# Optimization experiments

Hardware: AMD Instinct MI355X
Metric: run time of the kernel (lower is better)

The kernel has to match this reference:

```python
import jax, jax.numpy as jnp
import numpy as np

IH, IW = 32, 32
HEADS, DIM_HEAD = 8, 32
EPS = 1e-6


def conv3x3(x, w):
    # x: [B,C,H,W], w: [O,I,3,3], stride 1, pad 1, no bias
    return jax.lax.conv_general_dilated(x, w, (1, 1), ((1, 1), (1, 1)),
                                        dimension_numbers=('NCHW', 'OIHW', 'NCHW'))


def groupnorm1(x, g, b):
    # GroupNorm(1, C): normalize over (C,H,W) per sample
    mu = jnp.mean(x, axis=(1, 2, 3), keepdims=True)
    var = jnp.var(x, axis=(1, 2, 3), keepdims=True)
    xn = (x - mu) * jax.lax.rsqrt(var + EPS)
    return xn * g[None, :, None, None] + b[None, :, None, None]


def proj(x, w, g, b):
    return jax.nn.gelu(groupnorm1(conv3x3(x, w), g, b), approximate=False)


def relative_index(ih, iw):
    coords = np.stack(np.meshgrid(np.arange(ih), np.arange(iw), indexing='ij')).reshape(2, -1)
    rel = coords[:, :, None] - coords[:, None, :]  # [2, n, n]
    rel[0] += ih - 1
    rel[1] += iw - 1
    rel[0] *= 2 * iw - 1
    return jnp.asarray(rel.sum(0).reshape(-1))  # [n*n]


def setup_inputs() -> dict:
    key = jax.random.key(0)
    ks = jax.random.split(key, 9)
    C = HEADS * DIM_HEAD  # 256
    B = 8
    s = 0.02
    inp = {
        'x': jax.random.normal(ks[0], (B, C, IH, IW), jnp.float32),
        'wq': jax.random.normal(ks[1], (C, C, 3, 3), jnp.float32) * s,
        'wk': jax.random.normal(ks[2], (C, C, 3, 3), jnp.float32) * s,
        'wv': jax.random.normal(ks[3], (C, C, 3, 3), jnp.float32) * s,
        'gq': jnp.ones((C,), jnp.float32), 'bq': jnp.zeros((C,), jnp.float32),
        'gk': jnp.ones((C,), jnp.float32), 'bk': jnp.zeros((C,), jnp.float32),
        'gv': jnp.ones((C,), jnp.float32), 'bv': jnp.zeros((C,), jnp.float32),
        'bias_table': jax.random.normal(ks[4], ((2 * IH - 1) * (2 * IW - 1), HEADS), jnp.float32) * s,
        'wo': jax.random.normal(ks[5], (C, C), jnp.float32) * s,
        'bo': jnp.zeros((C,), jnp.float32),
    }
    return inp


def reference(x, wq, wk, wv, gq, bq, gk, bk, gv, bv, bias_table, wo, bo):
    B, C, ih, iw = x.shape
    n = ih * iw
    h, d = HEADS, DIM_HEAD

    q = proj(x, wq, gq, bq)  # [B,C,H,W]
    k = proj(x, wk, gk, bk)
    v = proj(x, wv, gv, bv)

    # 'b c ih iw -> b (ih iw) c' then 'b n (h d) -> b h n d'  ==  [B,h,d,n] -> [B,h,n,d]
    def to_heads(t):
        return t.reshape(B, h, d, n).transpose(0, 1, 3, 2)

    q4, k4, v4 = to_heads(q), to_heads(k), to_heads(v)

    # NOTE: original code applies self.scale only when y is not None; y=None here -> no scale.
    dots = jnp.einsum('bhnd,bhmd->bhnm', q4, k4)  # [B,h,n,n]

    rel_idx = relative_index(ih, iw)  # [n*n]
    rel_bias = bias_table[rel_idx].reshape(n, n, h).transpose(2, 0, 1)[None]  # [1,h,n,n]

    attn = jax.nn.softmax(dots + rel_bias, axis=-1)
    out = jnp.einsum('bhnm,bhmd->bhnd', attn, v4)  # [B,h,n,d]

    # 'b h n d -> b n (h d)' then 'b (ih iw) c -> b c ih iw'
    out = out.transpose(0, 2, 1, 3).reshape(B, n, C).transpose(0, 2, 1).reshape(B, C, ih, iw)

    # to_out: 1x1 conv with bias (dropout=0 in eval)
    out = jnp.einsum('oc,bchw->bohw', wo, out) + bo[None, :, None, None]
    return out
```

## Files before the change

kernel.cpp:

```cpp
#include <hip/hip_runtime.h>
#include <cstdint>
#include <cstddef>

#define GEPS 1e-6f

using bf16x8 = __attribute__((ext_vector_type(8))) short;
using f32x4  = __attribute__((ext_vector_type(4))) float;

__device__ inline ushort f2bf(float x) {
    union { float f; uint32_t u; } v; v.f = x;
    uint32_t r = (v.u + 0x7fffu + ((v.u >> 16) & 1u)) >> 16;
    return (ushort)r;
}
__device__ inline float bf2f(ushort b) {
    union { float f; uint32_t u; } v; v.u = ((uint32_t)b) << 16;
    return v.f;
}

__device__ inline void gll16(const void* g, void* l) {
    __builtin_amdgcn_global_load_lds(
        (const __attribute__((address_space(1))) void*)g,
        (__attribute__((address_space(3))) void*)l, 16, 0, 0);
}

__global__ __launch_bounds__(256) void prep_k(
    const float* __restrict__ x,
    const float* __restrict__ wq, const float* __restrict__ wk,
    const float* __restrict__ wv, const float* __restrict__ wo,
    const float* __restrict__ btab,
    ushort* __restrict__ Xcl, ushort* __restrict__ Wbuf,
    ushort* __restrict__ wo_bf, ushort* __restrict__ Bx)
{
    __shared__ __align__(16) ushort Xs[3 * 34 * 128];
    int tid = threadIdx.x;
    int blk = blockIdx.x;

    if (blk < 256) {
        int b = blk >> 5, y = blk & 31;
#pragma unroll
        for (int it = 0; it < 8; ++it) {
            int idx = it * 256 + tid;
            int ci = idx >> 3, pxg = idx & 7;
            float4 v = *(const float4*)&x[((size_t)(b * 256 + ci)) * 1024 + y * 32 + pxg * 4];
            int base = (pxg * 4) * 264 + ci;
            Xs[base + 0 * 264] = f2bf(v.x);
            Xs[base + 1 * 264] = f2bf(v.y);
            Xs[base + 2 * 264] = f2bf(v.z);
            Xs[base + 3 * 264] = f2bf(v.w);
        }
        __syncthreads();
        uint4 z4 = make_uint4(0u, 0u, 0u, 0u);
        ushort* orow = Xcl + ((size_t)(b * 34) + y + 1) * 34 * 256;
#pragma unroll
        for (int it = 0; it < 4; ++it) {
            int idx = it * 256 + tid;
            int px = idx >> 5, ci8 = idx & 31;
            *(uint4*)&orow[(px + 1) * 256 + ci8 * 8] =
                *(const uint4*)&Xs[px * 264 + ci8 * 8];
        }
        if (tid < 64) {
            int side = tid >> 5, ci8 = tid & 31;
            *(uint4*)&orow[side * 33 * 256 + ci8 * 8] = z4;
        }
        if (y == 0 || y == 31) {
            ushort* zrow = Xcl + ((size_t)(b * 34) + (y == 0 ? 0 : 33)) * 34 * 256;
#pragma unroll
            for (int it = 0; it < 5; ++it) {
                int idx = it * 256 + tid;
                if (idx < 1088) *(uint4*)&zrow[idx * 8] = z4;
            }
        }
        return;
    }
    if (blk < 1024) {
        int wrow = blk - 256;
        int proj = wrow >> 8, co = wrow & 255;
        const float* src = ((proj == 0) ? wq : ((proj == 1) ? wk : wv)) + (size_t)co * 2304;
#pragma unroll
        for (int j = 0; j < 9; ++j) {
            int idx = j * 256 + tid;
            Xs[idx] = f2bf(src[idx]);
        }
        __syncthreads();
        ushort* dst = Wbuf + (size_t)wrow * 2304;
#pragma unroll
        for (int j = 0; j < 9; ++j)
            dst[j * 256 + tid] = Xs[tid * 9 + j];
        return;
    }
    if (blk < 1088) {
        int t = (blk - 1024) * 256 + tid;
        float4 v = *(const float4*)&wo[(size_t)t * 4];
        union { uint2 u; ushort s[4]; } o;
        o.s[0] = f2bf(v.x); o.s[1] = f2bf(v.y); o.s[2] = f2bf(v.z); o.s[3] = f2bf(v.w);
        *(uint2*)&wo_bf[(size_t)t * 4] = o.u;
        return;
    }
    int g = (blk - 1088) * 4 + (tid >> 6);
    int l = tid & 63;
    int h = g >> 10, qt = (g >> 4) & 63, kt = g & 15;
    int quad = l >> 4, c = l & 15;
    union { uint4 v[2]; ushort s[16]; } o;
#pragma unroll
    for (int f = 0; f < 4; ++f)
#pragma unroll
        for (int r = 0; r < 4; ++r) {
            int qrow = qt * 16 + quad * 4 + r;
            int key = kt * 64 + f * 16 + c;
            int dy = (qrow >> 5) - (key >> 5) + 31;
            int dx = (qrow & 31) - (key & 31) + 31;
            o.s[f * 4 + r] = f2bf(btab[(dy * 63 + dx) * 8 + h]);
        }
    uint4* dst = (uint4*)(Bx + ((size_t)g * 64 + l) * 16);
    dst[0] = o.v[0];
    dst[1] = o.v[1];
}

__global__ __launch_bounds__(256, 3) void gemm_bt(
    const ushort* __restrict__ A, const ushort* __restrict__ B,
    int M, int N, int K,
    ushort* __restrict__ Cpart,
    float* __restrict__ Cout, const float* __restrict__ bias, int mode)
{
    __shared__ __align__(16) ushort As[128 * 64];
    __shared__ __align__(16) ushort Bs[128 * 64];
    int tid = threadIdx.x;
    int mbase = blockIdx.x * 128, nbase = blockIdx.y * 128;
    int kspan = K / gridDim.z;
    int k0 = blockIdx.z * kspan;
    int wave = tid >> 6, lane = tid & 63;
    int wm = wave & 1, wn = wave >> 1;
    int quad = lane >> 4, c = lane & 15;

    int row_s = tid >> 3;
    int cc8 = (tid & 7) ^ (row_s & 7);
    ushort* ldsA = As + wave * 512;
    ushort* ldsB = Bs + wave * 512;

    int rb[4];
    if (mode == 0) {
#pragma unroll
        for (int R = 0; R < 4; ++R) {
            int r = mbase + R * 32 + row_s;
            int b_ = r >> 10, yy = (r >> 5) & 31, xx = r & 31;
            rb[R] = ((b_ * 34 + yy) * 34 + xx) * 256;
        }
    }

    f32x4 acc[4][4];
#pragma unroll
    for (int i = 0; i < 4; ++i)
#pragma unroll
        for (int j = 0; j < 4; ++j) acc[i][j] = (f32x4){0.f, 0.f, 0.f, 0.f};

    for (int kb = k0; kb < k0 + kspan; kb += 64) {
        __syncthreads();
        if (mode == 0) {
            int tap = kb >> 8;
            int kh = (tap * 11) >> 5;
            int kw = tap - kh * 3;
            int toff = (kh * 34 + kw) * 256 + (kb & 255) + cc8 * 8;
#pragma unroll
            for (int R = 0; R < 4; ++R) {
                gll16(A + rb[R] + toff, ldsA + R * 2048);
                gll16(B + (size_t)(nbase + R * 32 + row_s) * K + kb + cc8 * 8,
                      ldsB + R * 2048);
            }
        } else {
#pragma unroll
            for (int R = 0; R < 4; ++R) {
                int row = R * 32 + row_s;
                gll16(A + (size_t)(mbase + row) * K + kb + cc8 * 8,
                      ldsA + R * 2048);
                gll16(B + (size_t)(nbase + row) * K + kb + cc8 * 8,
                      ldsB + R * 2048);
            }
        }
        __syncthreads();
#pragma unroll
        for (int kq = 0; kq < 2; ++kq) {
            bf16x8 af[4], bfr[4];
            int sw = ((kq * 4 + quad) ^ (c & 7)) * 8;
#pragma unroll
            for (int i = 0; i < 4; ++i) {
                af[i]  = *(const bf16x8*)&As[(wm * 64 + i * 16 + c) * 64 + sw];
                bfr[i] = *(const bf16x8*)&Bs[(wn * 64 + i * 16 + c) * 64 + sw];
            }
#pragma unroll
            for (int i = 0; i < 4; ++i)
#pragma unroll
                for (int j = 0; j < 4; ++j)
                    acc[i][j] = __builtin_amdgcn_mfma_f32_16x16x32_bf16(
                        af[i], bfr[j], acc[i][j], 0, 0, 0);
        }
    }

    if (mode == 0) {
        ushort* Cp = Cpart + (size_t)blockIdx.z * M * N;
#pragma unroll
        for (int i = 0; i < 4; ++i) {
            int mrow = mbase + wm * 64 + i * 16 + quad * 4;
#pragma unroll
            for (int j = 0; j < 4; ++j) {
                int ncol = nbase + wn * 64 + j * 16 + c;
#pragma unroll
                for (int r = 0; r < 4; ++r)
                    Cp[(size_t)(mrow + r) * N + ncol] = f2bf(acc[i][j][r]);
            }
        }
    } else {
#pragma unroll
        for (int i = 0; i < 4; ++i) {
            int mrow0 = mbase + wm * 64 + i * 16 + quad * 4;
#pragma unroll
            for (int j = 0; j < 4; ++j) {
                int ncol = nbase + wn * 64 + j * 16 + c;
                int bb = ncol >> 10, px = ncol & 1023;
#pragma unroll
                for (int r = 0; r < 4; ++r) {
                    int o = mrow0 + r;
                    Cout[((size_t)bb * 256 + o) * 1024 + px] = acc[i][j][r] + bias[o];
                }
            }
        }
    }
}

__global__ __launch_bounds__(256) void stats1_k(const ushort* __restrict__ P0,
                                                const ushort* __restrict__ P1,
                                                float2* __restrict__ part)
{
    int t = blockIdx.x * 256 + threadIdx.x;
    size_t base = (size_t)t * 8;
    union { uint4 v; ushort s[8]; } a, b2;
    a.v  = *(const uint4*)&P0[base];
    b2.v = *(const uint4*)&P1[base];
    float s1 = 0.f, s2 = 0.f;
#pragma unroll
    for (int e = 0; e < 8; ++e) {
        float v = bf2f(a.s[e]) + bf2f(b2.s[e]);
        s1 += v; s2 += v * v;
    }
#pragma unroll
    for (int mk = 1; mk < 32; mk <<= 1) {
        s1 += __shfl_xor(s1, mk, 64);
        s2 += __shfl_xor(s2, mk, 64);
    }
    if ((threadIdx.x & 31) == 0) {
        int gg = t >> 5;
        int m = gg / 3;
        int proj = gg - m * 3;
        int b = m >> 10, slot = m & 1023;
        part[(proj * 8 + b) * 1024 + slot] = make_float2(s1, s2);
    }
}

__global__ __launch_bounds__(256) void stats2_k(const float2* __restrict__ part,
                                                float* __restrict__ stats)
{
    __shared__ float w1[4], w2[4];
    int s = blockIdx.x, tid = threadIdx.x;
    float s1 = 0.f, s2 = 0.f;
#pragma unroll
    for (int i = 0; i < 4; ++i) {
        float2 v = part[(size_t)s * 1024 + tid * 4 + i];
        s1 += v.x; s2 += v.y;
    }
#pragma unroll
    for (int mk = 1; mk < 64; mk <<= 1) {
        s1 += __shfl_xor(s1, mk, 64);
        s2 += __shfl_xor(s2, mk, 64);
    }
    if ((tid & 63) == 0) { w1[tid >> 6] = s1; w2[tid >> 6] = s2; }
    __syncthreads();
    if (tid == 0) {
        stats[s * 2 + 0] = w1[0] + w1[1] + w1[2] + w1[3];
        stats[s * 2 + 1] = w2[0] + w2[1] + w2[2] + w2[3];
    }
}

__global__ void gn_k(const ushort* __restrict__ P0, const ushort* __restrict__ P1,
                     const float* __restrict__ stats,
                     const float* __restrict__ gq, const float* __restrict__ bq,
                     const float* __restrict__ gk, const float* __restrict__ bk,
                     const float* __restrict__ gv, const float* __restrict__ bv,
                     ushort* __restrict__ qb, ushort* __restrict__ kb2,
                     ushort* __restrict__ vx)
{
    int t = blockIdx.x * 256 + threadIdx.x;
    int m = t / 96;
    int nn = (t - m * 96) * 8;
    int proj = nn >> 8, co = nn & 255;
    int b = m >> 10, px = m & 1023;
    float s1 = stats[(proj * 8 + b) * 2 + 0];
    float s2 = stats[(proj * 8 + b) * 2 + 1];
    const float Ninv = 1.f / 262144.f;
    float mu = s1 * Ninv;
    float var = fmaxf(s2 * Ninv - mu * mu, 0.f);
    float rsig = rsqrtf(var + GEPS);
    const float* gam = (proj == 0) ? gq : ((proj == 1) ? gk : gv);
    const float* bet = (proj == 0) ? bq : ((proj == 1) ? bk : bv);

    size_t base = (size_t)m * 768 + nn;
    union { uint4 v; ushort s[8]; } a, c2;
    a.v  = *(const uint4*)&P0[base];
    c2.v = *(const uint4*)&P1[base];
    union { uint4 v; ushort s[8]; } outp;
#pragma unroll
    for (int e = 0; e < 8; ++e) {
        int cc = co + e;
        float xv = bf2f(a.s[e]) + bf2f(c2.s[e]);
        float xn = (xv - mu) * rsig * gam[cc] + bet[cc];
        float ge = 0.5f * xn * (1.f + erff(xn * 0.70710678118654752f));
        outp.s[e] = f2bf(ge);
    }
    int h = co >> 5, d = co & 31;
    if (proj == 0) {
        *(uint4*)(qb + ((((size_t)b * 8 + h) * 1024 + px) * 32 + d)) = outp.v;
    } else if (proj == 1) {
        *(uint4*)(kb2 + ((((size_t)b * 8 + h) * 1024 + px) * 32 + d)) = outp.v;
    } else {
        ushort* vb = vx + ((size_t)b * 8 + h) * 32768;
        int kca = px >> 5, quad = (px >> 3) & 3, j = px & 7;
#pragma unroll
        for (int e = 0; e < 8; ++e) {
            int dd = d + e;
            vb[(((kca * 2 + (dd >> 4)) * 64) + quad * 16 + (dd & 15)) * 8 + j] = outp.s[e];
        }
    }
}

__global__ __launch_bounds__(256, 8) void attn_k(
    const ushort* __restrict__ qb, const ushort* __restrict__ kb,
    const ushort* __restrict__ vx, const ushort* __restrict__ Bx,
    ushort* __restrict__ Opart, float* __restrict__ lpart)
{
    __shared__ __align__(16) ushort Pl[4 * 16 * 72];
    int tid = threadIdx.x, wave = tid >> 6, lane = tid & 63;
    int quad = lane >> 4, c = lane & 15;
    int bh = blockIdx.y;
    int h = bh & 7;
    int z = blockIdx.z;
    int qbase = blockIdx.x * 64 + wave * 16;

    const ushort* Q  = qb + (size_t)bh * 1024 * 32;
    const ushort* Kp = kb + (size_t)bh * 1024 * 32;
    const ushort* Vb = vx + (size_t)bh * 32768;
    const ushort* bxp = Bx + (((size_t)(h * 64 + (qbase >> 4)) * 16) * 64 + lane) * 16;
    ushort* Pw = Pl + wave * 16 * 72;

    bf16x8 qf = *(const bf16x8*)&Q[(qbase + c) * 32 + quad * 8];

    float l_[4] = {0.f, 0.f, 0.f, 0.f};
    f32x4 Of0 = {0.f, 0.f, 0.f, 0.f}, Of1 = {0.f, 0.f, 0.f, 0.f};

    for (int kb64 = z * 512; kb64 < z * 512 + 512; kb64 += 64) {
        f32x4 S[4];
        f32x4 zf = {0.f, 0.f, 0.f, 0.f};
#pragma unroll
        for (int f = 0; f < 4; ++f) {
            bf16x8 kf = *(const bf16x8*)&Kp[(kb64 + f * 16 + c) * 32 + quad * 8];
            S[f] = __builtin_amdgcn_mfma_f32_16x16x32_bf16(qf, kf, zf, 0, 0, 0);
        }
        union { uint4 v[2]; ushort s[16]; } bu;
        const uint4* bsrc = (const uint4*)(bxp + (size_t)(kb64 >> 6) * 1024);
        bu.v[0] = bsrc[0];
        bu.v[1] = bsrc[1];
#pragma unroll
        for (int f = 0; f < 4; ++f)
#pragma unroll
            for (int r = 0; r < 4; ++r) {
                float p = __expf(S[f][r] + bf2f(bu.s[f * 4 + r]));
                S[f][r] = p;
                l_[r] += p;
            }
#pragma unroll
        for (int f = 0; f < 4; ++f)
#pragma unroll
            for (int r = 0; r < 4; ++r)
                Pw[(quad * 4 + r) * 72 + f * 16 + c] = f2bf(S[f][r]);
#pragma unroll
        for (int kc = 0; kc < 2; ++kc) {
            int kca = (kb64 >> 5) + kc;
            bf16x8 pf = *(const bf16x8*)&Pw[c * 72 + kc * 32 + quad * 8];
            bf16x8 vf0 = *(const bf16x8*)&Vb[((kca * 2 + 0) * 64 + lane) * 8];
            Of0 = __builtin_amdgcn_mfma_f32_16x16x32_bf16(pf, vf0, Of0, 0, 0, 0);
            bf16x8 vf1 = *(const bf16x8*)&Vb[((kca * 2 + 1) * 64 + lane) * 8];
            Of1 = __builtin_amdgcn_mfma_f32_16x16x32_bf16(pf, vf1, Of1, 0, 0, 0);
        }
    }
#pragma unroll
    for (int r = 0; r < 4; ++r) {
        float l = l_[r];
        l += __shfl_xor(l, 1, 64);
        l += __shfl_xor(l, 2, 64);
        l += __shfl_xor(l, 4, 64);
        l += __shfl_xor(l, 8, 64);
        int qr = qbase + quad * 4 + r;
        size_t ob = (((size_t)z * 64 + bh) * 1024 + qr) * 32;
        Opart[ob + c]      = f2bf(Of0[r]);
        Opart[ob + 16 + c] = f2bf(Of1[r]);
        if (c == 0) lpart[(size_t)z * 65536 + bh * 1024 + qr] = l;
    }
}

__global__ __launch_bounds__(256) void combine_k(const ushort* __restrict__ Opart,
                                                 const float* __restrict__ lpart,
                                                 ushort* __restrict__ attnout)
{
    int t = blockIdx.x * 256 + threadIdx.x;
    int g = t & 3;
    int qg = t >> 2;
    int bh = qg >> 10, qr = qg & 1023;
    int b = bh >> 3, h = bh & 7;
    size_t ob = ((size_t)qg) * 32 + g * 8;
    union { uint4 v; ushort s[8]; } o0, o1;
    o0.v = *(const uint4*)&Opart[ob];
    o1.v = *(const uint4*)&Opart[(size_t)64 * 1024 * 32 + ob];
    float inv = 1.f / (lpart[qg] + lpart[65536 + qg]);
    union { uint4 u; ushort s[8]; } o;
#pragma unroll
    for (int e = 0; e < 8; ++e)
        o.s[e] = f2bf((bf2f(o0.s[e]) + bf2f(o1.s[e])) * inv);
    *(uint4*)&attnout[(((size_t)b * 1024 + qr) * 256) + h * 32 + g * 8] = o.u;
}

extern "C" void kernel_launch(void* const* d_in, const int* in_sizes, int n_in,
                              void* d_out, int out_size, void* d_ws, size_t ws_size,
                              hipStream_t stream)
{
    const float* x    = (const float*)d_in[0];
    const float* wq   = (const float*)d_in[1];
    const float* wk   = (const float*)d_in[2];
    const float* wv   = (const float*)d_in[3];
    const float* gq   = (const float*)d_in[4];
    const float* bq   = (const float*)d_in[5];
    const float* gk   = (const float*)d_in[6];
    const float* bk   = (const float*)d_in[7];
    const float* gv   = (const float*)d_in[8];
    const float* bv   = (const float*)d_in[9];
    const float* btab = (const float*)d_in[10];
    const float* wo   = (const float*)d_in[11];
    const float* bo   = (const float*)d_in[12];
    float* out = (float*)d_out;

    char* w = (char*)d_ws;
    size_t off = 0;
    auto alloc = [&](size_t bytes) -> char* {
        char* p = w + off;
        off += (bytes + 255) & ~(size_t)255;
        return p;
    };
    ushort* Xcl     = (ushort*)alloc(8ull * 34 * 34 * 256 * 2);
    ushort* Wbuf    = (ushort*)alloc(768ull * 2304 * 2);
    ushort* wo_bf   = (ushort*)alloc(65536ull * 2);
    ushort* Bx      = (ushort*)alloc(8192ull * 64 * 16 * 2);
    ushort* P0      = (ushort*)alloc(8192ull * 768 * 2);
    ushort* P1      = (ushort*)alloc(8192ull * 768 * 2);
    float2* part    = (float2*)alloc(48ull * 1024 * 8);
    float*  stats   = (float*)alloc(384);
    ushort* Opart   = (ushort*)alloc(2ull * 64 * 1024 * 32 * 2);
    float*  lpart   = (float*)alloc(2ull * 64 * 1024 * 4);
    ushort* qb      = (ushort*)alloc(8ull * 8 * 1024 * 32 * 2);
    ushort* kb2     = (ushort*)alloc(8ull * 8 * 1024 * 32 * 2);
    ushort* vx      = (ushort*)alloc(8ull * 8 * 32 * 1024 * 2);
    ushort* attnout = (ushort*)alloc(8ull * 1024 * 256 * 2);

    prep_k<<<3136, 256, 0, stream>>>(x, wq, wk, wv, wo, btab,
                                     Xcl, Wbuf, wo_bf, Bx);
    gemm_bt<<<dim3(64, 6, 2), 256, 0, stream>>>(Xcl, Wbuf, 8192, 768, 2304,
                                                P0, nullptr, nullptr, 0);
    stats1_k<<<3072, 256, 0, stream>>>(P0, P1, part);
    stats2_k<<<48, 256, 0, stream>>>(part, stats);
    gn_k<<<3072, 256, 0, stream>>>(P0, P1, stats, gq, bq, gk, bk, gv, bv,
                                   qb, kb2, vx);
    attn_k<<<dim3(16, 64, 2), 256, 0, stream>>>(qb, kb2, vx, Bx, Opart, lpart);
    combine_k<<<1024, 256, 0, stream>>>(Opart, lpart, attnout);
    gemm_bt<<<dim3(2, 64, 1), 256, 0, stream>>>(wo_bf, attnout, 256, 8192, 256,
                                                nullptr, out, bo, 1);
}
```

Measured before the change: 213.0 us.

## Drop split-K in conv GEMM and attention, fuse GroupNorm stats via atomics

The conv GEMM no longer splits K across two partial buffers. It uses a 128x64 tile with twice as many N blocks and accumulates GroupNorm sums with per-block atomics in its epilogue, which removes the stats1/stats2 kernels and the second partial read in gn_k. Attention no longer splits keys into two halves, so it normalizes and writes the final output directly and the combine kernel goes away. This cuts launches and intermediate traffic, at the cost of halving grid parallelism for attention and adding float atomics, which make the statistics order-dependent.

```diff
diff --git a/kernel.cpp b/kernel.cpp
--- a/kernel.cpp
+++ b/kernel.cpp
@@ -29,7 +29,8 @@
     const float* __restrict__ wv, const float* __restrict__ wo,
     const float* __restrict__ btab,
     ushort* __restrict__ Xcl, ushort* __restrict__ Wbuf,
-    ushort* __restrict__ wo_bf, ushort* __restrict__ Bx)
+    ushort* __restrict__ wo_bf, ushort* __restrict__ Bx,
+    float* __restrict__ stats)
 {
     __shared__ __align__(16) ushort Xs[3 * 34 * 128];
     int tid = threadIdx.x;
@@ -89,6 +90,7 @@
         return;
     }
     if (blk < 1088) {
+        if (blk == 1024 && tid < 192) stats[tid] = 0.f;
         int t = (blk - 1024) * 256 + tid;
         float4 v = *(const float4*)&wo[(size_t)t * 4];
         union { uint2 u; ushort s[4]; } o;
@@ -119,15 +121,14 @@
 __global__ __launch_bounds__(256, 3) void gemm_bt(
     const ushort* __restrict__ A, const ushort* __restrict__ B,
     int M, int N, int K,
-    ushort* __restrict__ Cpart,
+    ushort* __restrict__ Cpart, float* __restrict__ stats,
     float* __restrict__ Cout, const float* __restrict__ bias, int mode)
 {
     __shared__ __align__(16) ushort As[128 * 64];
-    __shared__ __align__(16) ushort Bs[128 * 64];
+    __shared__ __align__(16) ushort Bs[64 * 64];
+    __shared__ float red[8];
     int tid = threadIdx.x;
-    int mbase = blockIdx.x * 128, nbase = blockIdx.y * 128;
-    int kspan = K / gridDim.z;
-    int k0 = blockIdx.z * kspan;
+    int mbase = blockIdx.x * 128, nbase = blockIdx.y * 64;
     int wave = tid >> 6, lane = tid & 63;
     int wm = wave & 1, wn = wave >> 1;
     int quad = lane >> 4, c = lane & 15;
@@ -147,13 +148,13 @@
         }
     }
 
-    f32x4 acc[4][4];
+    f32x4 acc[4][2];
 #pragma unroll
     for (int i = 0; i < 4; ++i)
 #pragma unroll
-        for (int j = 0; j < 4; ++j) acc[i][j] = (f32x4){0.f, 0.f, 0.f, 0.f};
-
-    for (int kb = k0; kb < k0 + kspan; kb += 64) {
+        for (int j = 0; j < 2; ++j) acc[i][j] = (f32x4){0.f, 0.f, 0.f, 0.f};
+
+    for (int kb = 0; kb < K; kb += 64) {
         __syncthreads();
         if (mode == 0) {
             int tap = kb >> 8;
@@ -161,60 +162,77 @@
             int kw = tap - kh * 3;
             int toff = (kh * 34 + kw) * 256 + (kb & 255) + cc8 * 8;
 #pragma unroll
-            for (int R = 0; R < 4; ++R) {
+            for (int R = 0; R < 4; ++R)
                 gll16(A + rb[R] + toff, ldsA + R * 2048);
-                gll16(B + (size_t)(nbase + R * 32 + row_s) * K + kb + cc8 * 8,
-                      ldsB + R * 2048);
-            }
+#pragma unroll
+            for (int S = 0; S < 2; ++S)
+                gll16(B + (size_t)(nbase + S * 32 + row_s) * K + kb + cc8 * 8,
+                      ldsB + S * 2048);
         } else {
 #pragma unroll
-            for (int R = 0; R < 4; ++R) {
-                int row = R * 32 + row_s;
-                gll16(A + (size_t)(mbase + row) * K + kb + cc8 * 8,
+            for (int R = 0; R < 4; ++R)
+                gll16(A + (size_t)(mbase + R * 32 + row_s) * K + kb + cc8 * 8,
                       ldsA + R * 2048);
-                gll16(B + (size_t)(nbase + row) * K + kb + cc8 * 8,
-                      ldsB + R * 2048);
-            }
+#pragma unroll
+            for (int S = 0; S < 2; ++S)
+                gll16(B + (size_t)(nbase + S * 32 + row_s) * K + kb + cc8 * 8,
+                      ldsB + S * 2048);
         }
         __syncthreads();
 #pragma unroll
         for (int kq = 0; kq < 2; ++kq) {
-            bf16x8 af[4], bfr[4];
+            bf16x8 af[4], bfr[2];
             int sw = ((kq * 4 + quad) ^ (c & 7)) * 8;
 #pragma unroll
-            for (int i = 0; i < 4; ++i) {
+            for (int i = 0; i < 4; ++i)
                 af[i]  = *(const bf16x8*)&As[(wm * 64 + i * 16 + c) * 64 + sw];
-                bfr[i] = *(const bf16x8*)&Bs[(wn * 64 + i * 16 + c) * 64 + sw];
-            }
+#pragma unroll
+            for (int j = 0; j < 2; ++j)
+                bfr[j] = *(const bf16x8*)&Bs[(wn * 32 + j * 16 + c) * 64 + sw];
 #pragma unroll
             for (int i = 0; i < 4; ++i)
 #pragma unroll
-                for (int j = 0; j < 4; ++j)
+                for (int j = 0; j < 2; ++j)
                     acc[i][j] = __builtin_amdgcn_mfma_f32_16x16x32_bf16(
                         af[i], bfr[j], acc[i][j], 0, 0, 0);
         }
     }
 
     if (mode == 0) {
-        ushort* Cp = Cpart + (size_t)blockIdx.z * M * N;
+        float s1 = 0.f, s2 = 0.f;
 #pragma unroll
         for (int i = 0; i < 4; ++i) {
             int mrow = mbase + wm * 64 + i * 16 + quad * 4;
 #pragma unroll
-            for (int j = 0; j < 4; ++j) {
-                int ncol = nbase + wn * 64 + j * 16 + c;
-#pragma unroll
-                for (int r = 0; r < 4; ++r)
-                    Cp[(size_t)(mrow + r) * N + ncol] = f2bf(acc[i][j][r]);
+            for (int j = 0; j < 2; ++j) {
+                int ncol = nbase + wn * 32 + j * 16 + c;
+#pragma unroll
+                for (int r = 0; r < 4; ++r) {
+                    float v = acc[i][j][r];
+                    s1 += v; s2 += v * v;
+                    Cpart[(size_t)(mrow + r) * N + ncol] = f2bf(v);
+                }
             }
+        }
+#pragma unroll
+        for (int mk = 1; mk < 64; mk <<= 1) {
+            s1 += __shfl_xor(s1, mk, 64);
+            s2 += __shfl_xor(s2, mk, 64);
+        }
+        if (lane == 0) { red[wave] = s1; red[4 + wave] = s2; }
+        __syncthreads();
+        if (tid == 0) {
+            int key = (blockIdx.y >> 2) * 8 + (blockIdx.x >> 3);
+            atomicAdd(&stats[key * 2 + 0], red[0] + red[1] + red[2] + red[3]);
+            atomicAdd(&stats[key * 2 + 1], red[4] + red[5] + red[6] + red[7]);
         }
     } else {
 #pragma unroll
         for (int i = 0; i < 4; ++i) {
             int mrow0 = mbase + wm * 64 + i * 16 + quad * 4;
 #pragma unroll
-            for (int j = 0; j < 4; ++j) {
-                int ncol = nbase + wn * 64 + j * 16 + c;
+            for (int j = 0; j < 2; ++j) {
+                int ncol = nbase + wn * 32 + j * 16 + c;
                 int bb = ncol >> 10, px = ncol & 1023;
 #pragma unroll
                 for (int r = 0; r < 4; ++r) {
@@ -226,60 +244,7 @@
     }
 }
 
-__global__ __launch_bounds__(256) void stats1_k(const ushort* __restrict__ P0,
-                                                const ushort* __restrict__ P1,
-                                                float2* __restrict__ part)
-{
-    int t = blockIdx.x * 256 + threadIdx.x;
-    size_t base = (size_t)t * 8;
-    union { uint4 v; ushort s[8]; } a, b2;
-    a.v  = *(const uint4*)&P0[base];
-    b2.v = *(const uint4*)&P1[base];
-    float s1 = 0.f, s2 = 0.f;
-#pragma unroll
-    for (int e = 0; e < 8; ++e) {
-        float v = bf2f(a.s[e]) + bf2f(b2.s[e]);
-        s1 += v; s2 += v * v;
-    }
-#pragma unroll
-    for (int mk = 1; mk < 32; mk <<= 1) {
-        s1 += __shfl_xor(s1, mk, 64);
-        s2 += __shfl_xor(s2, mk, 64);
-    }
-    if ((threadIdx.x & 31) == 0) {
-        int gg = t >> 5;
-        int m = gg / 3;
-        int proj = gg - m * 3;
-        int b = m >> 10, slot = m & 1023;
-        part[(proj * 8 + b) * 1024 + slot] = make_float2(s1, s2);
-    }
-}
-
-__global__ __launch_bounds__(256) void stats2_k(const float2* __restrict__ part,
-                                                float* __restrict__ stats)
-{
-    __shared__ float w1[4], w2[4];
-    int s = blockIdx.x, tid = threadIdx.x;
-    float s1 = 0.f, s2 = 0.f;
-#pragma unroll
-    for (int i = 0; i < 4; ++i) {
-        float2 v = part[(size_t)s * 1024 + tid * 4 + i];
-        s1 += v.x; s2 += v.y;
-    }
-#pragma unroll
-    for (int mk = 1; mk < 64; mk <<= 1) {
-        s1 += __shfl_xor(s1, mk, 64);
-        s2 += __shfl_xor(s2, mk, 64);
-    }
-    if ((tid & 63) == 0) { w1[tid >> 6] = s1; w2[tid >> 6] = s2; }
-    __syncthreads();
-    if (tid == 0) {
-        stats[s * 2 + 0] = w1[0] + w1[1] + w1[2] + w1[3];
-        stats[s * 2 + 1] = w2[0] + w2[1] + w2[2] + w2[3];
-    }
-}
-
-__global__ void gn_k(const ushort* __restrict__ P0, const ushort* __restrict__ P1,
+__global__ void gn_k(const ushort* __restrict__ P0,
                      const float* __restrict__ stats,
                      const float* __restrict__ gq, const float* __restrict__ bq,
                      const float* __restrict__ gk, const float* __restrict__ bk,
@@ -302,14 +267,13 @@
     const float* bet = (proj == 0) ? bq : ((proj == 1) ? bk : bv);
 
     size_t base = (size_t)m * 768 + nn;
-    union { uint4 v; ushort s[8]; } a, c2;
-    a.v  = *(const uint4*)&P0[base];
-    c2.v = *(const uint4*)&P1[base];
+    union { uint4 v; ushort s[8]; } a;
+    a.v = *(const uint4*)&P0[base];
     union { uint4 v; ushort s[8]; } outp;
 #pragma unroll
     for (int e = 0; e < 8; ++e) {
         int cc = co + e;
-        float xv = bf2f(a.s[e]) + bf2f(c2.s[e]);
+        float xv = bf2f(a.s[e]);
         float xn = (xv - mu) * rsig * gam[cc] + bet[cc];
         float ge = 0.5f * xn * (1.f + erff(xn * 0.70710678118654752f));
         outp.s[e] = f2bf(ge);
@@ -333,14 +297,13 @@
 __global__ __launch_bounds__(256, 8) void attn_k(
     const ushort* __restrict__ qb, const ushort* __restrict__ kb,
     const ushort* __restrict__ vx, const ushort* __restrict__ Bx,
-    ushort* __restrict__ Opart, float* __restrict__ lpart)
+    ushort* __restrict__ attnout)
 {
     __shared__ __align__(16) ushort Pl[4 * 16 * 72];
     int tid = threadIdx.x, wave = tid >> 6, lane = tid & 63;
     int quad = lane >> 4, c = lane & 15;
     int bh = blockIdx.y;
     int h = bh & 7;
-    int z = blockIdx.z;
     int qbase = blockIdx.x * 64 + wave * 16;
 
     const ushort* Q  = qb + (size_t)bh * 1024 * 32;
@@ -354,7 +317,7 @@
     float l_[4] = {0.f, 0.f, 0.f, 0.f};
     f32x4 Of0 = {0.f, 0.f, 0.f, 0.f}, Of1 = {0.f, 0.f, 0.f, 0.f};
 
-    for (int kb64 = z * 512; kb64 < z * 512 + 512; kb64 += 64) {
+    for (int kb64 = 0; kb64 < 1024; kb64 += 64) {
         f32x4 S[4];
         f32x4 zf = {0.f, 0.f, 0.f, 0.f};
 #pragma unroll
@@ -389,6 +352,7 @@
             Of1 = __builtin_amdgcn_mfma_f32_16x16x32_bf16(pf, vf1, Of1, 0, 0, 0);
         }
     }
+    int b = bh >> 3;
 #pragma unroll
     for (int r = 0; r < 4; ++r) {
         float l = l_[r];
@@ -396,33 +360,12 @@
         l += __shfl_xor(l, 2, 64);
         l += __shfl_xor(l, 4, 64);
         l += __shfl_xor(l, 8, 64);
+        float inv = 1.f / l;
         int qr = qbase + quad * 4 + r;
-        size_t ob = (((size_t)z * 64 + bh) * 1024 + qr) * 32;
-        Opart[ob + c]      = f2bf(Of0[r]);
-        Opart[ob + 16 + c] = f2bf(Of1[r]);
-        if (c == 0) lpart[(size_t)z * 65536 + bh * 1024 + qr] = l;
-    }
-}
-
-__global__ __launch_bounds__(256) void combine_k(const ushort* __restrict__ Opart,
-                                                 const float* __restrict__ lpart,
-                                                 ushort* __restrict__ attnout)
-{
-    int t = blockIdx.x * 256 + threadIdx.x;
-    int g = t & 3;
-    int qg = t >> 2;
-    int bh = qg >> 10, qr = qg & 1023;
-    int b = bh >> 3, h = bh & 7;
-    size_t ob = ((size_t)qg) * 32 + g * 8;
-    union { uint4 v; ushort s[8]; } o0, o1;
-    o0.v = *(const uint4*)&Opart[ob];
-    o1.v = *(const uint4*)&Opart[(size_t)64 * 1024 * 32 + ob];
-    float inv = 1.f / (lpart[qg] + lpart[65536 + qg]);
-    union { uint4 u; ushort s[8]; } o;
-#pragma unroll
-    for (int e = 0; e < 8; ++e)
-        o.s[e] = f2bf((bf2f(o0.s[e]) + bf2f(o1.s[e])) * inv);
-    *(uint4*)&attnout[(((size_t)b * 1024 + qr) * 256) + h * 32 + g * 8] = o.u;
+        ushort* dst = attnout + ((size_t)b * 1024 + qr) * 256 + h * 32;
+        dst[c]      = f2bf(Of0[r] * inv);
+        dst[16 + c] = f2bf(Of1[r] * inv);
+    }
 }
 
 extern "C" void kernel_launch(void* const* d_in, const int* in_sizes, int n_in,
@@ -456,26 +399,19 @@
     ushort* wo_bf   = (ushort*)alloc(65536ull * 2);
     ushort* Bx      = (ushort*)alloc(8192ull * 64 * 16 * 2);
     ushort* P0      = (ushort*)alloc(8192ull * 768 * 2);
-    ushort* P1      = (ushort*)alloc(8192ull * 768 * 2);
-    float2* part    = (float2*)alloc(48ull * 1024 * 8);
-    float*  stats   = (float*)alloc(384);
-    ushort* Opart   = (ushort*)alloc(2ull * 64 * 1024 * 32 * 2);
-    float*  lpart   = (float*)alloc(2ull * 64 * 1024 * 4);
+    float*  stats   = (float*)alloc(768);
     ushort* qb      = (ushort*)alloc(8ull * 8 * 1024 * 32 * 2);
     ushort* kb2     = (ushort*)alloc(8ull * 8 * 1024 * 32 * 2);
     ushort* vx      = (ushort*)alloc(8ull * 8 * 32 * 1024 * 2);
     ushort* attnout = (ushort*)alloc(8ull * 1024 * 256 * 2);
 
     prep_k<<<3136, 256, 0, stream>>>(x, wq, wk, wv, wo, btab,
-                                     Xcl, Wbuf, wo_bf, Bx);
-    gemm_bt<<<dim3(64, 6, 2), 256, 0, stream>>>(Xcl, Wbuf, 8192, 768, 2304,
-                                                P0, nullptr, nullptr, 0);
-    stats1_k<<<3072, 256, 0, stream>>>(P0, P1, part);
-    stats2_k<<<48, 256, 0, stream>>>(part, stats);
-    gn_k<<<3072, 256, 0, stream>>>(P0, P1, stats, gq, bq, gk, bk, gv, bv,
+                                     Xcl, Wbuf, wo_bf, Bx, stats);
+    gemm_bt<<<dim3(64, 12, 1), 256, 0, stream>>>(Xcl, Wbuf, 8192, 768, 2304,
+                                                 P0, stats, nullptr, nullptr, 0);
+    gn_k<<<3072, 256, 0, stream>>>(P0, stats, gq, bq, gk, bk, gv, bv,
                                    qb, kb2, vx);
-    attn_k<<<dim3(16, 64, 2), 256, 0, stream>>>(qb, kb2, vx, Bx, Opart, lpart);
-    combine_k<<<1024, 256, 0, stream>>>(Opart, lpart, attnout);
-    gemm_bt<<<dim3(2, 64, 1), 256, 0, stream>>>(wo_bf, attnout, 256, 8192, 256,
-                                                nullptr, out, bo, 1);
-}
+    attn_k<<<dim3(16, 64, 1), 256, 0, stream>>>(qb, kb2, vx, Bx, attnout);
+    gemm_bt<<<dim3(2, 128, 1), 256, 0, stream>>>(wo_bf, attnout, 256, 8192, 256,
+                                                 nullptr, nullptr, out, bo, 1);
+}
```

Result: slower. 230.2 us (+8.1%).

## Index relative-position bias from LDS table, fuse GN stats via atomics, narrow out-proj tiles

Applied to the files above, without the earlier changes.

Replaces the precomputed expanded bias tensor (8 heads x 1024x1024 bf16) with a compact per-head bf16 bias table. Each attention block loads the table into LDS and indexes it by relative offset. This removes a large bias write in prep and the matching global reads in attention. GroupNorm statistics are accumulated with atomics into a buffer zeroed in prep, which drops the second reduction kernel. The output-projection GEMM is templated to a narrower N tile, doubling its grid for better occupancy. The trade-offs are atomic contention, nondeterministic summation order, and possible LDS bank conflicts on the bias lookups.

```diff
diff --git a/kernel.cpp b/kernel.cpp
--- a/kernel.cpp
+++ b/kernel.cpp
@@ -29,7 +29,8 @@
     const float* __restrict__ wv, const float* __restrict__ wo,
     const float* __restrict__ btab,
     ushort* __restrict__ Xcl, ushort* __restrict__ Wbuf,
-    ushort* __restrict__ wo_bf, ushort* __restrict__ Bx)
+    ushort* __restrict__ wo_bf, ushort* __restrict__ btab_bf,
+    float* __restrict__ stats)
 {
     __shared__ __align__(16) ushort Xs[3 * 34 * 128];
     int tid = threadIdx.x;
@@ -89,6 +90,7 @@
         return;
     }
     if (blk < 1088) {
+        if (blk == 1024 && tid < 192) stats[tid] = 0.f;
         int t = (blk - 1024) * 256 + tid;
         float4 v = *(const float4*)&wo[(size_t)t * 4];
         union { uint2 u; ushort s[4]; } o;
@@ -96,36 +98,26 @@
         *(uint2*)&wo_bf[(size_t)t * 4] = o.u;
         return;
     }
-    int g = (blk - 1088) * 4 + (tid >> 6);
-    int l = tid & 63;
-    int h = g >> 10, qt = (g >> 4) & 63, kt = g & 15;
-    int quad = l >> 4, c = l & 15;
-    union { uint4 v[2]; ushort s[16]; } o;
-#pragma unroll
-    for (int f = 0; f < 4; ++f)
-#pragma unroll
-        for (int r = 0; r < 4; ++r) {
-            int qrow = qt * 16 + quad * 4 + r;
-            int key = kt * 64 + f * 16 + c;
-            int dy = (qrow >> 5) - (key >> 5) + 31;
-            int dx = (qrow & 31) - (key & 31) + 31;
-            o.s[f * 4 + r] = f2bf(btab[(dy * 63 + dx) * 8 + h]);
-        }
-    uint4* dst = (uint4*)(Bx + ((size_t)g * 64 + l) * 16);
-    dst[0] = o.v[0];
-    dst[1] = o.v[1];
-}
-
+    int idx = (blk - 1088) * 256 + tid;
+    if (idx < 31752) {
+        int h = idx / 3969;
+        int j = idx - h * 3969;
+        btab_bf[h * 4096 + j] = f2bf(btab[(size_t)j * 8 + h]);
+    }
+}
+
+template<int NF>
 __global__ __launch_bounds__(256, 3) void gemm_bt(
     const ushort* __restrict__ A, const ushort* __restrict__ B,
     int M, int N, int K,
     ushort* __restrict__ Cpart,
     float* __restrict__ Cout, const float* __restrict__ bias, int mode)
 {
+    constexpr int BN = NF * 32;
     __shared__ __align__(16) ushort As[128 * 64];
-    __shared__ __align__(16) ushort Bs[128 * 64];
+    __shared__ __align__(16) ushort Bs[BN * 64];
     int tid = threadIdx.x;
-    int mbase = blockIdx.x * 128, nbase = blockIdx.y * 128;
+    int mbase = blockIdx.x * 128, nbase = blockIdx.y * BN;
     int kspan = K / gridDim.z;
     int k0 = blockIdx.z * kspan;
     int wave = tid >> 6, lane = tid & 63;
@@ -147,11 +139,11 @@
         }
     }
 
-    f32x4 acc[4][4];
+    f32x4 acc[4][NF];
 #pragma unroll
     for (int i = 0; i < 4; ++i)
 #pragma unroll
-        for (int j = 0; j < 4; ++j) acc[i][j] = (f32x4){0.f, 0.f, 0.f, 0.f};
+        for (int j = 0; j < NF; ++j) acc[i][j] = (f32x4){0.f, 0.f, 0.f, 0.f};
 
     for (int kb = k0; kb < k0 + kspan; kb += 64) {
         __syncthreads();
@@ -161,35 +153,37 @@
             int kw = tap - kh * 3;
             int toff = (kh * 34 + kw) * 256 + (kb & 255) + cc8 * 8;
 #pragma unroll
-            for (int R = 0; R < 4; ++R) {
+            for (int R = 0; R < 4; ++R)
                 gll16(A + rb[R] + toff, ldsA + R * 2048);
-                gll16(B + (size_t)(nbase + R * 32 + row_s) * K + kb + cc8 * 8,
-                      ldsB + R * 2048);
-            }
+#pragma unroll
+            for (int S = 0; S < NF; ++S)
+                gll16(B + (size_t)(nbase + S * 32 + row_s) * K + kb + cc8 * 8,
+                      ldsB + S * 2048);
         } else {
 #pragma unroll
-            for (int R = 0; R < 4; ++R) {
-                int row = R * 32 + row_s;
-                gll16(A + (size_t)(mbase + row) * K + kb + cc8 * 8,
+            for (int R = 0; R < 4; ++R)
+                gll16(A + (size_t)(mbase + R * 32 + row_s) * K + kb + cc8 * 8,
                       ldsA + R * 2048);
-                gll16(B + (size_t)(nbase + row) * K + kb + cc8 * 8,
-                      ldsB + R * 2048);
-            }
+#pragma unroll
+            for (int S = 0; S < NF; ++S)
+                gll16(B + (size_t)(nbase + S * 32 + row_s) * K + kb + cc8 * 8,
+                      ldsB + S * 2048);
         }
         __syncthreads();
 #pragma unroll
         for (int kq = 0; kq < 2; ++kq) {
-            bf16x8 af[4], bfr[4];
+            bf16x8 af[4], bfr[NF];
             int sw = ((kq * 4 + quad) ^ (c & 7)) * 8;
 #pragma unroll
-            for (int i = 0; i < 4; ++i) {
+            for (int i = 0; i < 4; ++i)
                 af[i]  = *(const bf16x8*)&As[(wm * 64 + i * 16 + c) * 64 + sw];
-                bfr[i] = *(const bf16x8*)&Bs[(wn * 64 + i * 16 + c) * 64 + sw];
-            }
+#pragma unroll
+            for (int j = 0; j < NF; ++j)
+                bfr[j] = *(const bf16x8*)&Bs[(wn * (NF * 16) + j * 16 + c) * 64 + sw];
 #pragma unroll
             for (int i = 0; i < 4; ++i)
 #pragma unroll
-                for (int j = 0; j < 4; ++j)
+                for (int j = 0; j < NF; ++j)
                     acc[i][j] = __builtin_amdgcn_mfma_f32_16x16x32_bf16(
                         af[i], bfr[j], acc[i][j], 0, 0, 0);
         }
@@ -201,8 +195,8 @@
         for (int i = 0; i < 4; ++i) {
             int mrow = mbase + wm * 64 + i * 16 + quad * 4;
 #pragma unroll
-            for (int j = 0; j < 4; ++j) {
-                int ncol = nbase + wn * 64 + j * 16 + c;
+            for (int j = 0; j < NF; ++j) {
+                int ncol = nbase + wn * (NF * 16) + j * 16 + c;
 #pragma unroll
                 for (int r = 0; r < 4; ++r)
                     Cp[(size_t)(mrow + r) * N + ncol] = f2bf(acc[i][j][r]);
@@ -213,8 +207,8 @@
         for (int i = 0; i < 4; ++i) {
             int mrow0 = mbase + wm * 64 + i * 16 + quad * 4;
 #pragma unroll
-            for (int j = 0; j < 4; ++j) {
-                int ncol = nbase + wn * 64 + j * 16 + c;
+            for (int j = 0; j < NF; ++j) {
+                int ncol = nbase + wn * (NF * 16) + j * 16 + c;
                 int bb = ncol >> 10, px = ncol & 1023;
 #pragma unroll
                 for (int r = 0; r < 4; ++r) {
@@ -228,7 +222,7 @@
 
 __global__ __launch_bounds__(256) void stats1_k(const ushort* __restrict__ P0,
                                                 const ushort* __restrict__ P1,
-                                                float2* __restrict__ part)
+                                                float* __restrict__ stats)
 {
     int t = blockIdx.x * 256 + threadIdx.x;
     size_t base = (size_t)t * 8;
@@ -250,32 +244,9 @@
         int gg = t >> 5;
         int m = gg / 3;
         int proj = gg - m * 3;
-        int b = m >> 10, slot = m & 1023;
-        part[(proj * 8 + b) * 1024 + slot] = make_float2(s1, s2);
-    }
-}
-
-__global__ __launch_bounds__(256) void stats2_k(const float2* __restrict__ part,
-                                                float* __restrict__ stats)
-{
-    __shared__ float w1[4], w2[4];
-    int s = blockIdx.x, tid = threadIdx.x;
-    float s1 = 0.f, s2 = 0.f;
-#pragma unroll
-    for (int i = 0; i < 4; ++i) {
-        float2 v = part[(size_t)s * 1024 + tid * 4 + i];
-        s1 += v.x; s2 += v.y;
-    }
-#pragma unroll
-    for (int mk = 1; mk < 64; mk <<= 1) {
-        s1 += __shfl_xor(s1, mk, 64);
-        s2 += __shfl_xor(s2, mk, 64);
-    }
-    if ((tid & 63) == 0) { w1[tid >> 6] = s1; w2[tid >> 6] = s2; }
-    __syncthreads();
-    if (tid == 0) {
-        stats[s * 2 + 0] = w1[0] + w1[1] + w1[2] + w1[3];
-        stats[s * 2 + 1] = w2[0] + w2[1] + w2[2] + w2[3];
+        int b = m >> 10;
+        atomicAdd(&stats[(proj * 8 + b) * 2 + 0], s1);
+        atomicAdd(&stats[(proj * 8 + b) * 2 + 1], s2);
     }
 }
 
@@ -332,10 +303,11 @@
 
 __global__ __launch_bounds__(256, 8) void attn_k(
     const ushort* __restrict__ qb, const ushort* __restrict__ kb,
-    const ushort* __restrict__ vx, const ushort* __restrict__ Bx,
+    const ushort* __restrict__ vx, const ushort* __restrict__ btab_bf,
     ushort* __restrict__ Opart, float* __restrict__ lpart)
 {
     __shared__ __align__(16) ushort Pl[4 * 16 * 72];
+    __shared__ __align__(16) ushort Bh[4096];
     int tid = threadIdx.x, wave = tid >> 6, lane = tid & 63;
     int quad = lane >> 4, c = lane & 15;
     int bh = blockIdx.y;
@@ -346,10 +318,22 @@
     const ushort* Q  = qb + (size_t)bh * 1024 * 32;
     const ushort* Kp = kb + (size_t)bh * 1024 * 32;
     const ushort* Vb = vx + (size_t)bh * 32768;
-    const ushort* bxp = Bx + (((size_t)(h * 64 + (qbase >> 4)) * 16) * 64 + lane) * 16;
     ushort* Pw = Pl + wave * 16 * 72;
 
+    {
+        const ushort* src = btab_bf + (h << 12);
+#pragma unroll
+        for (int rr = 0; rr < 2; ++rr)
+            gll16(src + (rr * 256 + tid) * 8, Bh + (rr * 256 + wave * 64) * 8);
+    }
+
     bf16x8 qf = *(const bf16x8*)&Q[(qbase + c) * 32 + quad * 8];
+
+    int qy = qbase >> 5;
+    int qx0 = (qbase & 31) + quad * 4;
+    int bb = (qy + 31 - z * 16) * 63 + qx0 + 31 - c;
+
+    __syncthreads();
 
     float l_[4] = {0.f, 0.f, 0.f, 0.f};
     f32x4 Of0 = {0.f, 0.f, 0.f, 0.f}, Of1 = {0.f, 0.f, 0.f, 0.f};
@@ -362,18 +346,17 @@
             bf16x8 kf = *(const bf16x8*)&Kp[(kb64 + f * 16 + c) * 32 + quad * 8];
             S[f] = __builtin_amdgcn_mfma_f32_16x16x32_bf16(qf, kf, zf, 0, 0, 0);
         }
-        union { uint4 v[2]; ushort s[16]; } bu;
-        const uint4* bsrc = (const uint4*)(bxp + (size_t)(kb64 >> 6) * 1024);
-        bu.v[0] = bsrc[0];
-        bu.v[1] = bsrc[1];
-#pragma unroll
-        for (int f = 0; f < 4; ++f)
+#pragma unroll
+        for (int f = 0; f < 4; ++f) {
+            int ao = bb - (f >> 1) * 63 - (f & 1) * 16;
 #pragma unroll
             for (int r = 0; r < 4; ++r) {
-                float p = __expf(S[f][r] + bf2f(bu.s[f * 4 + r]));
+                float p = __expf(S[f][r] + bf2f(Bh[ao + r]));
                 S[f][r] = p;
                 l_[r] += p;
             }
+        }
+        bb -= 126;
 #pragma unroll
         for (int f = 0; f < 4; ++f)
 #pragma unroll
@@ -454,11 +437,10 @@
     ushort* Xcl     = (ushort*)alloc(8ull * 34 * 34 * 256 * 2);
     ushort* Wbuf    = (ushort*)alloc(768ull * 2304 * 2);
     ushort* wo_bf   = (ushort*)alloc(65536ull * 2);
-    ushort* Bx      = (ushort*)alloc(8192ull * 64 * 16 * 2);
-    ushort* P0      = (ushort*)alloc(8192ull * 768 * 2);
-    ushort* P1      = (ushort*)alloc(8192ull * 768 * 2);
-    float2* part    = (float2*)alloc(48ull * 1024 * 8);
-    float*  stats   = (float*)alloc(384);
+    ushort* btab_bf = (ushort*)alloc(8ull * 4096 * 2);
+    ushort* P0      = (ushort*)alloc(2ull * 8192 * 768 * 2);
+    ushort* P1      = P0 + 8192ull * 768;
+    float*  stats   = (float*)alloc(768);
     ushort* Opart   = (ushort*)alloc(2ull * 64 * 1024 * 32 * 2);
     float*  lpart   = (float*)alloc(2ull * 64 * 1024 * 4);
     ushort* qb      = (ushort*)alloc(8ull * 8 * 1024 * 32 * 2);
@@ -466,16 +448,15 @@
     ushort* vx      = (ushort*)alloc(8ull * 8 * 32 * 1024 * 2);
     ushort* attnout = (ushort*)alloc(8ull * 1024 * 256 * 2);
 
-    prep_k<<<3136, 256, 0, stream>>>(x, wq, wk, wv, wo, btab,
-                                     Xcl, Wbuf, wo_bf, Bx);
-    gemm_bt<<<dim3(64, 6, 2), 256, 0, stream>>>(Xcl, Wbuf, 8192, 768, 2304,
-                                                P0, nullptr, nullptr, 0);
-    stats1_k<<<3072, 256, 0, stream>>>(P0, P1, part);
-    stats2_k<<<48, 256, 0, stream>>>(part, stats);
+    prep_k<<<1213, 256, 0, stream>>>(x, wq, wk, wv, wo, btab,
+                                     Xcl, Wbuf, wo_bf, btab_bf, stats);
+    gemm_bt<4><<<dim3(64, 6, 2), 256, 0, stream>>>(Xcl, Wbuf, 8192, 768, 2304,
+                                                   P0, nullptr, nullptr, 0);
+    stats1_k<<<3072, 256, 0, stream>>>(P0, P1, stats);
     gn_k<<<3072, 256, 0, stream>>>(P0, P1, stats, gq, bq, gk, bk, gv, bv,
                                    qb, kb2, vx);
-    attn_k<<<dim3(16, 64, 2), 256, 0, stream>>>(qb, kb2, vx, Bx, Opart, lpart);
+    attn_k<<<dim3(16, 64, 2), 256, 0, stream>>>(qb, kb2, vx, btab_bf, Opart, lpart);
     combine_k<<<1024, 256, 0, stream>>>(Opart, lpart, attnout);
-    gemm_bt<<<dim3(2, 64, 1), 256, 0, stream>>>(wo_bf, attnout, 256, 8192, 256,
-                                                nullptr, out, bo, 1);
-}
+    gemm_bt<2><<<dim3(2, 128, 1), 256, 0, stream>>>(wo_bf, attnout, 256, 8192, 256,
+                                                    nullptr, out, bo, 1);
+}
```

After: 510.1 us. +139.5%, slower.
